# Kernel optimization log

Hardware: AMD Instinct MI355X
Metric: run time of the kernel (lower is better)

The kernel has to match this reference:

```python
import jax, jax.numpy as jnp
import numpy as np

ENC, DEC, B, S = 1024, 1024, 32, 2048


def setup_inputs() -> dict:
    key = jax.random.key(0)
    k1, k2, k3, k4, k5, k6 = jax.random.split(key, 6)
    scale_attn = 1.0 / np.sqrt(ENC + DEC)
    return {
        "decoder_hidden": jax.random.normal(k1, (B, DEC), dtype=jnp.float32),
        "encoder_outputs": jax.random.normal(k2, (B, S, ENC), dtype=jnp.float32),
        "mask": jax.random.randint(k3, (B, S), 0, 2, dtype=jnp.int32),
        "W_attn": jax.random.normal(k4, (ENC + DEC, DEC), dtype=jnp.float32) * scale_attn,
        "b_attn": jax.random.normal(k5, (DEC,), dtype=jnp.float32) * 0.02,
        "v_w": jax.random.normal(k6, (DEC,), dtype=jnp.float32) * (1.0 / np.sqrt(DEC)),
    }


def reference(decoder_hidden, encoder_outputs, mask, W_attn, b_attn, v_w):
    # Split cat((dec_exp, enc)) @ W into two GEMMs (same math, no repeat/concat).
    dec_dim = decoder_hidden.shape[-1]
    W_dec = W_attn[:dec_dim]      # [DEC, DEC]
    W_enc = W_attn[dec_dim:]      # [ENC, DEC]
    dec_proj = decoder_hidden @ W_dec                      # [B, DEC]
    enc_proj = jnp.einsum("bse,ed->bsd", encoder_outputs, W_enc)  # [B, S, DEC]
    energy = jnp.tanh(dec_proj[:, None, :] + enc_proj + b_attn)   # [B, S, DEC]
    scores = jnp.einsum("bsd,d->bs", energy, v_w)                 # [B, S]
    scores = jnp.where(mask == 0, -1e9, scores)
    attn_weights = jax.nn.softmax(scores, axis=1)                 # [B, S]
    context = jnp.einsum("bs,bse->be", attn_weights, encoder_outputs)  # [B, ENC]
    return (context, attn_weights)
```

## Files before the change

kernel.cpp:

```cpp
#include <hip/hip_runtime.h>
#include <hip/hip_bf16.h>
#include <cstdint>


#define ENCD 1024
#define DECD 1024
#define BATCH 32
#define SEQ 2048
#define MTOT (BATCH * SEQ)
#define KDIM 1024
#define NDIM 1024

typedef __attribute__((ext_vector_type(4))) float f32x4;
typedef __attribute__((ext_vector_type(8))) __bf16 bf16x8;
typedef __attribute__((ext_vector_type(8))) unsigned short u16x8;

__device__ __forceinline__ unsigned short f2bf(float f) {
  unsigned int u = __builtin_bit_cast(unsigned int, f);
  u += 0x7fffu + ((u >> 16) & 1u);
  return (unsigned short)(u >> 16);
}

__device__ __forceinline__ float bf2f(unsigned short h) {
  return __builtin_bit_cast(float, (unsigned int)h << 16);
}

__device__ __forceinline__ void async_lds16(const unsigned short* g, unsigned short* l) {
  __builtin_amdgcn_global_load_lds(
      (const __attribute__((address_space(1))) unsigned int*)g,
      (__attribute__((address_space(3))) unsigned int*)l, 16, 0, 0);
}

__global__ void conv_bf16_k(const float* __restrict__ src, unsigned short* __restrict__ dst) {
  const long i = ((long)blockIdx.x * 256 + threadIdx.x) * 8;
  const f32x4 f0 = *(const f32x4*)(src + i);
  const f32x4 f1 = *(const f32x4*)(src + i + 4);
  u16x8 v;
  v[0] = f2bf(f0[0]); v[1] = f2bf(f0[1]); v[2] = f2bf(f0[2]); v[3] = f2bf(f0[3]);
  v[4] = f2bf(f1[0]); v[5] = f2bf(f1[1]); v[6] = f2bf(f1[2]); v[7] = f2bf(f1[3]);
  *(u16x8*)(dst + i) = v;
}

__global__ void wt_k(const float* __restrict__ W, unsigned short* __restrict__ Wt) {
  __shared__ unsigned short t[64][65];
  const int k0 = blockIdx.x * 64, n0 = blockIdx.y * 64;
  const int tx = threadIdx.x & 63, ty = threadIdx.x >> 6;
#pragma unroll
  for (int i = 0; i < 16; ++i) {
    const int k = ty + i * 4;
    t[k][tx] = f2bf(W[(long)(DECD + k0 + k) * NDIM + n0 + tx]);
  }
  __syncthreads();
#pragma unroll
  for (int i = 0; i < 16; ++i) {
    const int n = ty + i * 4;
    Wt[(long)(n0 + n) * KDIM + k0 + tx] = t[tx][n];
  }
}

__global__ void dec1_k(const float* __restrict__ dec, const float* __restrict__ W,
                       float* __restrict__ part) {
  const int idx = blockIdx.x * 256 + threadIdx.x;
  const int kc = blockIdx.y;
  const int b = idx >> 10;
  const int n = idx & 1023;
  const float* d = dec + b * DECD + kc * 128;
  const float* w = W + (long)(kc * 128) * NDIM + n;
  float acc = 0.f;
#pragma unroll 8
  for (int k = 0; k < 128; ++k) acc = fmaf(d[k], w[(long)k * NDIM], acc);
  part[kc * 32768 + idx] = acc;
}

__global__ void dec2_k(const float* __restrict__ part, const float* __restrict__ bias,
                       float* __restrict__ dp) {
  const int idx = blockIdx.x * 256 + threadIdx.x;
  float s = bias[idx & 1023];
#pragma unroll
  for (int kc = 0; kc < 8; ++kc) s += part[kc * 32768 + idx];
  dp[idx] = s;
}

__global__ __launch_bounds__(256, 4) void gemm_fast(
    const unsigned short* __restrict__ Abf, const unsigned short* __restrict__ Wt,
    const float* __restrict__ dp, const float* __restrict__ vw,
    float* __restrict__ sp) {
  __shared__ unsigned short sA[128 * 64];
  __shared__ unsigned short sB[128 * 64];

  const int tid = threadIdx.x;
  const int lane = tid & 63;
  const int wave = tid >> 6;
  const int wm = wave >> 1, wn = wave & 1;
  const int quad = lane >> 4;
  const int l15 = lane & 15;

  const int bn = blockIdx.x;
  const int bm = blockIdx.y;
  const int n0 = bn * 128;
  const int row0 = bm * 128;
  const int bidx = bm >> 4;

  const int srow = lane >> 3;
  const int schunk = (lane & 7) ^ srow;

  const f32x4 zz = {0.f, 0.f, 0.f, 0.f};
  f32x4 acc[4][4];
#pragma unroll
  for (int i = 0; i < 4; ++i)
#pragma unroll
    for (int j = 0; j < 4; ++j) acc[i][j] = zz;

  for (int kt = 0; kt < 16; ++kt) {
    const int k0 = kt * 64;
    __syncthreads();
#pragma unroll
    for (int i = 0; i < 4; ++i) {
      const int r = wave * 32 + i * 8 + srow;
      async_lds16(Abf + (size_t)(row0 + r) * KDIM + k0 + schunk * 8,
                  &sA[(wave * 32 + i * 8) * 64]);
      async_lds16(Wt + (size_t)(n0 + r) * KDIM + k0 + schunk * 8,
                  &sB[(wave * 32 + i * 8) * 64]);
    }
    __syncthreads();
#pragma unroll
    for (int h = 0; h < 2; ++h) {
      bf16x8 af[4], bf[4];
      const int slot = ((h * 4 + quad) ^ (l15 & 7)) * 8;
#pragma unroll
      for (int t = 0; t < 4; ++t) {
        af[t] = __builtin_bit_cast(bf16x8, *(const u16x8*)&sA[(wm * 64 + t * 16 + l15) * 64 + slot]);
        bf[t] = __builtin_bit_cast(bf16x8, *(const u16x8*)&sB[(wn * 64 + t * 16 + l15) * 64 + slot]);
      }
#pragma unroll
      for (int mt = 0; mt < 4; ++mt)
#pragma unroll
        for (int nt = 0; nt < 4; ++nt)
          acc[mt][nt] = __builtin_amdgcn_mfma_f32_16x16x32_bf16(
              af[mt], bf[nt], acc[mt][nt], 0, 0, 0);
    }
  }

  float vv[4], dv[4];
#pragma unroll
  for (int nt = 0; nt < 4; ++nt) {
    const int n = n0 + wn * 64 + nt * 16 + l15;
    vv[nt] = vw[n];
    dv[nt] = dp[bidx * NDIM + n];
  }
  float s_arr[4][4];
#pragma unroll
  for (int mt = 0; mt < 4; ++mt) {
#pragma unroll
    for (int r = 0; r < 4; ++r) {
      float s = 0.f;
#pragma unroll
      for (int nt = 0; nt < 4; ++nt) {
        float x = acc[mt][nt][r] + dv[nt];
        x = fminf(fmaxf(x, -10.f), 10.f);
        const float e = __expf(2.f * x);
        s += (e - 1.f) * __builtin_amdgcn_rcpf(e + 1.f) * vv[nt];
      }
      s += __shfl_xor(s, 1);
      s += __shfl_xor(s, 2);
      s += __shfl_xor(s, 4);
      s += __shfl_xor(s, 8);
      s_arr[mt][r] = s;
    }
  }
  __syncthreads();
  float* sRed = (float*)sA;
  if (wn == 1 && l15 == 0) {
#pragma unroll
    for (int mt = 0; mt < 4; ++mt)
#pragma unroll
      for (int r = 0; r < 4; ++r)
        sRed[wm * 64 + mt * 16 + quad * 4 + r] = s_arr[mt][r];
  }
  __syncthreads();
  if (wn == 0 && l15 == 0) {
#pragma unroll
    for (int mt = 0; mt < 4; ++mt)
#pragma unroll
      for (int r = 0; r < 4; ++r) {
        const int ml = wm * 64 + mt * 16 + quad * 4 + r;
        sp[(size_t)bn * MTOT + row0 + ml] = s_arr[mt][r] + sRed[ml];
      }
  }
}

__global__ void softmax_part_k(const float* __restrict__ sp, const int* __restrict__ mask,
                               float* __restrict__ attn) {
  const int b = blockIdx.x;
  const int tid = threadIdx.x;
  const int w = tid >> 6;
  __shared__ float redm[4], reds[4];
  const int* mrow = mask + b * SEQ;
  float vals[8];
  float mx = -3.0e38f;
#pragma unroll
  for (int i = 0; i < 8; ++i) {
    const int s = tid + i * 256;
    float v = 0.f;
#pragma unroll
    for (int bn = 0; bn < 8; ++bn) v += sp[(size_t)bn * MTOT + b * SEQ + s];
    if (mrow[s] == 0) v = -1.0e9f;
    vals[i] = v;
    mx = fmaxf(mx, v);
  }
#pragma unroll
  for (int off = 1; off < 64; off <<= 1) mx = fmaxf(mx, __shfl_xor(mx, off));
  if ((tid & 63) == 0) redm[w] = mx;
  __syncthreads();
  mx = fmaxf(fmaxf(redm[0], redm[1]), fmaxf(redm[2], redm[3]));
  float sum = 0.f;
#pragma unroll
  for (int i = 0; i < 8; ++i) {
    vals[i] = __expf(vals[i] - mx);
    sum += vals[i];
  }
#pragma unroll
  for (int off = 1; off < 64; off <<= 1) sum += __shfl_xor(sum, off);
  if ((tid & 63) == 0) reds[w] = sum;
  __syncthreads();
  sum = reds[0] + reds[1] + reds[2] + reds[3];
  const float inv = 1.0f / sum;
#pragma unroll
  for (int i = 0; i < 8; ++i) attn[b * SEQ + tid + i * 256] = vals[i] * inv;
}

__global__ void ctx1_k(const float* __restrict__ attn, const unsigned short* __restrict__ Abf,
                       float* __restrict__ part) {
  const int sc = blockIdx.x;
  const int b = blockIdx.y;
  const int e0 = threadIdx.x * 8;
  const float* arow = attn + b * SEQ + sc * 128;
  const unsigned short* base = Abf + (size_t)(b * SEQ + sc * 128) * ENCD + e0;
  float acc[8] = {0.f, 0.f, 0.f, 0.f, 0.f, 0.f, 0.f, 0.f};
#pragma unroll 8
  for (int s = 0; s < 128; ++s) {
    const float w = arow[s];
    const u16x8 v = *(const u16x8*)(base + (size_t)s * ENCD);
#pragma unroll
    for (int j = 0; j < 8; ++j) acc[j] = fmaf(w, bf2f(v[j]), acc[j]);
  }
  float* dst = part + (size_t)sc * (BATCH * ENCD) + b * ENCD + e0;
  *(f32x4*)dst = *(f32x4*)&acc[0];
  *(f32x4*)(dst + 4) = *(f32x4*)&acc[4];
}

__global__ void ctx2_k(const float* __restrict__ part, float* __restrict__ ctx) {
  const int i = blockIdx.x * 256 + threadIdx.x;
  float s = 0.f;
#pragma unroll
  for (int c = 0; c < 16; ++c) s += part[(size_t)c * (BATCH * ENCD) + i];
  ctx[i] = s;
}

__global__ void dec_proj_k2(const float* __restrict__ dec, const float* __restrict__ W,
                            float* __restrict__ dp) {
  const int idx = blockIdx.x * 256 + threadIdx.x;
  const int kc = blockIdx.y;
  const int b = idx >> 10;
  const int n = idx & 1023;
  const float* d = dec + b * DECD + kc * 128;
  const float* w = W + (long)(kc * 128) * NDIM + n;
  float acc = 0.f;
#pragma unroll 8
  for (int k = 0; k < 128; ++k) acc = fmaf(d[k], w[(long)k * NDIM], acc);
  atomicAdd(&dp[idx], acc);
}

__global__ __launch_bounds__(256, 3) void gemm_scores_bf16(
    const unsigned short* __restrict__ Abf, const unsigned short* __restrict__ Wt,
    const float* __restrict__ dp, const float* __restrict__ bias,
    const float* __restrict__ vw, float* __restrict__ scores) {
  __shared__ unsigned short sA[128 * 64];
  __shared__ unsigned short sB[128 * 64];
  const int tid = threadIdx.x;
  const int lane = tid & 63;
  const int wave = tid >> 6;
  const int wm = wave >> 1, wn = wave & 1;
  const int quad = lane >> 4;
  const int l15 = lane & 15;
  const int bn = blockIdx.x, bm = blockIdx.y;
  const int n0 = bn * 128, row0 = bm * 128, bidx = bm >> 4;
  const int srow = lane >> 3;
  const int schunk = (lane & 7) ^ srow;
  const f32x4 zz = {0.f, 0.f, 0.f, 0.f};
  f32x4 acc[4][4];
#pragma unroll
  for (int i = 0; i < 4; ++i)
#pragma unroll
    for (int j = 0; j < 4; ++j) acc[i][j] = zz;
  for (int kt = 0; kt < 16; ++kt) {
    const int k0 = kt * 64;
    __syncthreads();
#pragma unroll
    for (int i = 0; i < 4; ++i) {
      const int r = wave * 32 + i * 8 + srow;
      async_lds16(Abf + (size_t)(row0 + r) * KDIM + k0 + schunk * 8,
                  &sA[(wave * 32 + i * 8) * 64]);
      async_lds16(Wt + (size_t)(n0 + r) * KDIM + k0 + schunk * 8,
                  &sB[(wave * 32 + i * 8) * 64]);
    }
    __syncthreads();
#pragma unroll
    for (int h = 0; h < 2; ++h) {
      bf16x8 af[4], bf[4];
      const int slot = ((h * 4 + quad) ^ (l15 & 7)) * 8;
#pragma unroll
      for (int t = 0; t < 4; ++t) {
        af[t] = __builtin_bit_cast(bf16x8, *(const u16x8*)&sA[(wm * 64 + t * 16 + l15) * 64 + slot]);
        bf[t] = __builtin_bit_cast(bf16x8, *(const u16x8*)&sB[(wn * 64 + t * 16 + l15) * 64 + slot]);
      }
#pragma unroll
      for (int mt = 0; mt < 4; ++mt)
#pragma unroll
        for (int nt = 0; nt < 4; ++nt)
          acc[mt][nt] = __builtin_amdgcn_mfma_f32_16x16x32_bf16(
              af[mt], bf[nt], acc[mt][nt], 0, 0, 0);
    }
  }
  float vv[4], dv[4];
#pragma unroll
  for (int nt = 0; nt < 4; ++nt) {
    const int n = n0 + wn * 64 + nt * 16 + l15;
    vv[nt] = vw[n];
    dv[nt] = dp[bidx * NDIM + n] + bias[n];
  }
#pragma unroll
  for (int mt = 0; mt < 4; ++mt) {
#pragma unroll
    for (int r = 0; r < 4; ++r) {
      float s = 0.f;
#pragma unroll
      for (int nt = 0; nt < 4; ++nt) {
        float x = acc[mt][nt][r] + dv[nt];
        x = fminf(fmaxf(x, -10.f), 10.f);
        const float e = __expf(2.f * x);
        s += (e - 1.f) * __builtin_amdgcn_rcpf(e + 1.f) * vv[nt];
      }
      s += __shfl_xor(s, 1);
      s += __shfl_xor(s, 2);
      s += __shfl_xor(s, 4);
      s += __shfl_xor(s, 8);
      if (l15 == 0) atomicAdd(&scores[row0 + wm * 64 + mt * 16 + quad * 4 + r], s);
    }
  }
}

__global__ __launch_bounds__(256, 2) void gemm_scores_f32(
    const float* __restrict__ Ag, const unsigned short* __restrict__ Wt,
    const float* __restrict__ dp, const float* __restrict__ bias,
    const float* __restrict__ vw, float* __restrict__ scores) {
  __shared__ unsigned short sA[128 * 64];
  __shared__ unsigned short sB[128 * 64];
  const int tid = threadIdx.x;
  const int lane = tid & 63;
  const int wave = tid >> 6;
  const int wm = wave >> 1, wn = wave & 1;
  const int quad = lane >> 4;
  const int l15 = lane & 15;
  const int bn = blockIdx.x, bm = blockIdx.y;
  const int n0 = bn * 128, row0 = bm * 128, bidx = bm >> 4;
  const int sr = tid >> 3, sc = tid & 7;
  const f32x4 zz = {0.f, 0.f, 0.f, 0.f};
  f32x4 acc[4][4];
#pragma unroll
  for (int i = 0; i < 4; ++i)
#pragma unroll
    for (int j = 0; j < 4; ++j) acc[i][j] = zz;
  for (int kt = 0; kt < 16; ++kt) {
    const int k0 = kt * 64;
    __syncthreads();
#pragma unroll
    for (int j = 0; j < 4; ++j) {
      const int r = sr + 32 * j;
      const int c = sc ^ (r & 7);
      const float* src = Ag + (long)(row0 + r) * KDIM + (k0 + c * 8);
      f32x4 f0 = *(const f32x4*)src;
      f32x4 f1 = *(const f32x4*)(src + 4);
      u16x8 v;
      v[0] = f2bf(f0[0]); v[1] = f2bf(f0[1]); v[2] = f2bf(f0[2]); v[3] = f2bf(f0[3]);
      v[4] = f2bf(f1[0]); v[5] = f2bf(f1[1]); v[6] = f2bf(f1[2]); v[7] = f2bf(f1[3]);
      *(u16x8*)&sA[r * 64 + sc * 8] = v;
      *(u16x8*)&sB[r * 64 + sc * 8] = *(const u16x8*)(Wt + (long)(n0 + r) * KDIM + (k0 + c * 8));
    }
    __syncthreads();
#pragma unroll
    for (int h = 0; h < 2; ++h) {
      const int cs = ((h * 4 + quad) ^ (lane & 7)) * 8;
      bf16x8 af[4], bf[4];
#pragma unroll
      for (int t = 0; t < 4; ++t) {
        af[t] = __builtin_bit_cast(bf16x8, *(const u16x8*)&sA[(wm * 64 + t * 16 + l15) * 64 + cs]);
        bf[t] = __builtin_bit_cast(bf16x8, *(const u16x8*)&sB[(wn * 64 + t * 16 + l15) * 64 + cs]);
      }
#pragma unroll
      for (int mt = 0; mt < 4; ++mt)
#pragma unroll
        for (int nt = 0; nt < 4; ++nt)
          acc[mt][nt] = __builtin_amdgcn_mfma_f32_16x16x32_bf16(
              af[mt], bf[nt], acc[mt][nt], 0, 0, 0);
    }
  }
  float vv[4], dv[4];
#pragma unroll
  for (int nt = 0; nt < 4; ++nt) {
    const int n = n0 + wn * 64 + nt * 16 + l15;
    vv[nt] = vw[n];
    dv[nt] = dp[bidx * NDIM + n] + bias[n];
  }
#pragma unroll
  for (int mt = 0; mt < 4; ++mt) {
#pragma unroll
    for (int r = 0; r < 4; ++r) {
      float s = 0.f;
#pragma unroll
      for (int nt = 0; nt < 4; ++nt) {
        float x = acc[mt][nt][r] + dv[nt];
        x = fminf(fmaxf(x, -10.f), 10.f);
        const float e = __expf(2.f * x);
        s += (e - 1.f) * __builtin_amdgcn_rcpf(e + 1.f) * vv[nt];
      }
      s += __shfl_xor(s, 1);
      s += __shfl_xor(s, 2);
      s += __shfl_xor(s, 4);
      s += __shfl_xor(s, 8);
      if (l15 == 0) atomicAdd(&scores[row0 + wm * 64 + mt * 16 + quad * 4 + r], s);
    }
  }
}

__global__ void softmax_k(float* __restrict__ sc, const int* __restrict__ mask) {
  const int b = blockIdx.x;
  const int tid = threadIdx.x;
  const int w = tid >> 6;
  __shared__ float redm[4], reds[4];
  float* row = sc + b * SEQ;
  const int* mrow = mask + b * SEQ;
  float vals[8];
  float mx = -3.0e38f;
#pragma unroll
  for (int i = 0; i < 8; ++i) {
    const int s = tid + i * 256;
    float v = row[s];
    if (mrow[s] == 0) v = -1.0e9f;
    vals[i] = v;
    mx = fmaxf(mx, v);
  }
#pragma unroll
  for (int off = 1; off < 64; off <<= 1) mx = fmaxf(mx, __shfl_xor(mx, off));
  if ((tid & 63) == 0) redm[w] = mx;
  __syncthreads();
  mx = fmaxf(fmaxf(redm[0], redm[1]), fmaxf(redm[2], redm[3]));
  float sum = 0.f;
#pragma unroll
  for (int i = 0; i < 8; ++i) {
    vals[i] = __expf(vals[i] - mx);
    sum += vals[i];
  }
#pragma unroll
  for (int off = 1; off < 64; off <<= 1) sum += __shfl_xor(sum, off);
  if ((tid & 63) == 0) reds[w] = sum;
  __syncthreads();
  sum = reds[0] + reds[1] + reds[2] + reds[3];
  const float inv = 1.0f / sum;
#pragma unroll
  for (int i = 0; i < 8; ++i) row[tid + i * 256] = vals[i] * inv;
}

__global__ void context_k(const float* __restrict__ attn, const float* __restrict__ enc,
                          float* __restrict__ ctx) {
  const int b = blockIdx.y;
  const int s0 = blockIdx.x * 32;
  const int e = threadIdx.x * 4;
  const float* arow = attn + b * SEQ + s0;
  const float* ebase = enc + (long)(b * SEQ + s0) * ENCD + e;
  f32x4 acc = {0.f, 0.f, 0.f, 0.f};
#pragma unroll 8
  for (int s = 0; s < 32; ++s) {
    const float w = arow[s];
    const f32x4 v = *(const f32x4*)(ebase + (long)s * ENCD);
    acc += w * v;
  }
  float* dst = ctx + b * ENCD + e;
  atomicAdd(dst + 0, acc[0]);
  atomicAdd(dst + 1, acc[1]);
  atomicAdd(dst + 2, acc[2]);
  atomicAdd(dst + 3, acc[3]);
}

extern "C" void kernel_launch(void* const* d_in, const int* in_sizes, int n_in,
                              void* d_out, int out_size, void* d_ws, size_t ws_size,
                              hipStream_t stream) {
  (void)in_sizes; (void)n_in; (void)out_size;
  const float* dec  = (const float*)d_in[0];
  const float* enc  = (const float*)d_in[1];
  const int*   mask = (const int*)d_in[2];
  const float* W    = (const float*)d_in[3];
  const float* bias = (const float*)d_in[4];
  const float* vw   = (const float*)d_in[5];

  float* ctx  = (float*)d_out;
  float* attn = (float*)d_out + BATCH * ENCD;
  unsigned short* Wt  = (unsigned short*)d_ws;
  unsigned short* Abf = (unsigned short*)((char*)d_ws + (2ull << 20));
  float* shared = (float*)((char*)d_ws + (130ull << 20));

  const size_t needA = (132ull << 20);
  const size_t needB = (2ull << 20) + ((size_t)MTOT * KDIM * 2);

  wt_k<<<dim3(16, 16), 256, 0, stream>>>(W, Wt);
  if (ws_size >= needA) {
    dec1_k<<<dim3(128, 8), 256, 0, stream>>>(dec, W, shared);
    dec2_k<<<128, 256, 0, stream>>>(shared, bias, ctx);
    conv_bf16_k<<<32768, 256, 0, stream>>>(enc, Abf);
    gemm_fast<<<dim3(8, 512), 256, 0, stream>>>(Abf, Wt, ctx, vw, shared);
    softmax_part_k<<<32, 256, 0, stream>>>(shared, mask, attn);
    ctx1_k<<<dim3(16, 32), 128, 0, stream>>>(attn, Abf, shared);
    ctx2_k<<<128, 256, 0, stream>>>(shared, ctx);
  } else if (ws_size >= needB) {
    hipMemsetAsync(attn, 0, (size_t)MTOT * sizeof(float), stream);
    hipMemsetAsync(ctx, 0, (size_t)(BATCH * NDIM) * sizeof(float), stream);
    dec_proj_k2<<<dim3(128, 8), 256, 0, stream>>>(dec, W, ctx);
    conv_bf16_k<<<32768, 256, 0, stream>>>(enc, Abf);
    gemm_scores_bf16<<<dim3(8, 512), 256, 0, stream>>>(Abf, Wt, ctx, bias, vw, attn);
    softmax_k<<<32, 256, 0, stream>>>(attn, mask);
    hipMemsetAsync(ctx, 0, (size_t)(BATCH * ENCD) * sizeof(float), stream);
    context_k<<<dim3(64, 32), 256, 0, stream>>>(attn, enc, ctx);
  } else {
    hipMemsetAsync(attn, 0, (size_t)MTOT * sizeof(float), stream);
    hipMemsetAsync(ctx, 0, (size_t)(BATCH * NDIM) * sizeof(float), stream);
    dec_proj_k2<<<dim3(128, 8), 256, 0, stream>>>(dec, W, ctx);
    gemm_scores_f32<<<dim3(8, 512), 256, 0, stream>>>(enc, Wt, ctx, bias, vw, attn);
    softmax_k<<<32, 256, 0, stream>>>(attn, mask);
    hipMemsetAsync(ctx, 0, (size_t)(BATCH * ENCD) * sizeof(float), stream);
    context_k<<<dim3(64, 32), 256, 0, stream>>>(attn, enc, ctx);
  }
}
```

Before: 572.6 us.

## Use 256x256 double-buffered 8-wave GEMM tile with interleaved async loads

Replaces the 128x128 single-buffered GEMM with a 256x256 tile run by 8 waves. It double-buffers LDS and interleaves async global-to-LDS loads with MFMA phases, using explicit vmcnt waits and s_setprio. This is meant to hide load latency, which the old loop exposed behind __syncthreads, and to halve the global re-reads of A and W. The larger tile uses 128KB of LDS and more accumulator registers, which limits occupancy. Separately, ctx1_k is split across two halves of the sequence per block to raise parallelism.

After: 595.8 us. 1.04x slower.

```diff
diff --git a/kernel.cpp b/kernel.cpp
--- a/kernel.cpp
+++ b/kernel.cpp
@@ -29,6 +29,22 @@
   __builtin_amdgcn_global_load_lds(
       (const __attribute__((address_space(1))) unsigned int*)g,
       (__attribute__((address_space(3))) unsigned int*)l, 16, 0, 0);
+}
+
+__device__ __forceinline__ void barx() {
+  __builtin_amdgcn_s_barrier();
+  asm volatile("" ::: "memory");
+}
+
+template <int N>
+__device__ __forceinline__ void waitv() {
+  if constexpr (N == 0) {
+    asm volatile("s_waitcnt vmcnt(0)" ::: "memory");
+  } else if constexpr (N == 2) {
+    asm volatile("s_waitcnt vmcnt(2)" ::: "memory");
+  } else {
+    asm volatile("s_waitcnt vmcnt(4)" ::: "memory");
+  }
 }
 
 __global__ void conv_bf16_k(const float* __restrict__ src, unsigned short* __restrict__ dst) {
@@ -81,65 +97,159 @@
   dp[idx] = s;
 }
 
-__global__ __launch_bounds__(256, 4) void gemm_fast(
+template <bool STG, int W1, int W2>
+__device__ __forceinline__ void gtile(
+    const unsigned short* Acur, const unsigned short* Bcur,
+    unsigned short* Anxt, unsigned short* Bnxt,
+    const unsigned short* Ab, const unsigned short* Bb, int k0n,
+    int wm, int wn, int wv, int quad, int l15, int srow, int schunk,
+    f32x4 (&acc)[8][4], bf16x8 (&aF)[4][2], bf16x8 (&bF)[4][2]) {
+  const int sw = l15 & 7;
+#define RDF(buf, row, h) \
+  __builtin_bit_cast(bf16x8, *(const u16x8*)&(buf)[(row) * 64 + ((((h) * 4 + quad) ^ sw) * 8)])
+#pragma unroll
+  for (int mt = 0; mt < 4; ++mt) {
+    const int row = wm * 128 + mt * 16 + l15;
+    aF[mt][0] = RDF(Acur, row, 0);
+    aF[mt][1] = RDF(Acur, row, 1);
+  }
+#pragma unroll
+  for (int nt = 0; nt < 2; ++nt) {
+    const int row = wn * 64 + nt * 16 + l15;
+    bF[nt][0] = RDF(Bcur, row, 0);
+    bF[nt][1] = RDF(Bcur, row, 1);
+  }
+  if (STG) {
+    async_lds16(Bb + (size_t)(wv * 16 + srow) * KDIM + k0n + schunk * 8, Bnxt + (wv * 16) * 64);
+    async_lds16(Bb + (size_t)(wv * 16 + 8 + srow) * KDIM + k0n + schunk * 8, Bnxt + (wv * 16 + 8) * 64);
+  }
+  barx();
+  __builtin_amdgcn_s_setprio(1);
+#pragma unroll
+  for (int h = 0; h < 2; ++h)
+#pragma unroll
+    for (int mt = 0; mt < 4; ++mt)
+#pragma unroll
+      for (int nt = 0; nt < 2; ++nt)
+        acc[mt][nt] = __builtin_amdgcn_mfma_f32_16x16x32_bf16(aF[mt][h], bF[nt][h], acc[mt][nt], 0, 0, 0);
+  __builtin_amdgcn_s_setprio(0);
+  barx();
+#pragma unroll
+  for (int nt = 2; nt < 4; ++nt) {
+    const int row = wn * 64 + nt * 16 + l15;
+    bF[nt][0] = RDF(Bcur, row, 0);
+    bF[nt][1] = RDF(Bcur, row, 1);
+  }
+  if (STG) {
+    async_lds16(Bb + (size_t)(128 + wv * 16 + srow) * KDIM + k0n + schunk * 8, Bnxt + (128 + wv * 16) * 64);
+    async_lds16(Bb + (size_t)(128 + wv * 16 + 8 + srow) * KDIM + k0n + schunk * 8, Bnxt + (128 + wv * 16 + 8) * 64);
+  }
+  waitv<W1>();
+  barx();
+  __builtin_amdgcn_s_setprio(1);
+#pragma unroll
+  for (int h = 0; h < 2; ++h)
+#pragma unroll
+    for (int mt = 0; mt < 4; ++mt)
+#pragma unroll
+      for (int nt = 0; nt < 2; ++nt)
+        acc[mt][2 + nt] = __builtin_amdgcn_mfma_f32_16x16x32_bf16(aF[mt][h], bF[2 + nt][h], acc[mt][2 + nt], 0, 0, 0);
+  __builtin_amdgcn_s_setprio(0);
+  barx();
+#pragma unroll
+  for (int mt = 0; mt < 4; ++mt) {
+    const int row = wm * 128 + (4 + mt) * 16 + l15;
+    aF[mt][0] = RDF(Acur, row, 0);
+    aF[mt][1] = RDF(Acur, row, 1);
+  }
+  if (STG) {
+    async_lds16(Ab + (size_t)(wv * 8 + srow) * KDIM + k0n + schunk * 8, Anxt + (wv * 8) * 64);
+    async_lds16(Ab + (size_t)(128 + wv * 8 + srow) * KDIM + k0n + schunk * 8, Anxt + (128 + wv * 8) * 64);
+  }
+  barx();
+  __builtin_amdgcn_s_setprio(1);
+#pragma unroll
+  for (int h = 0; h < 2; ++h)
+#pragma unroll
+    for (int mt = 0; mt < 4; ++mt)
+#pragma unroll
+      for (int nt = 0; nt < 2; ++nt)
+        acc[4 + mt][nt] = __builtin_amdgcn_mfma_f32_16x16x32_bf16(aF[mt][h], bF[nt][h], acc[4 + mt][nt], 0, 0, 0);
+  __builtin_amdgcn_s_setprio(0);
+  barx();
+  if (STG) {
+    async_lds16(Ab + (size_t)(64 + wv * 8 + srow) * KDIM + k0n + schunk * 8, Anxt + (64 + wv * 8) * 64);
+    async_lds16(Ab + (size_t)(192 + wv * 8 + srow) * KDIM + k0n + schunk * 8, Anxt + (192 + wv * 8) * 64);
+  }
+  waitv<W2>();
+  barx();
+  __builtin_amdgcn_s_setprio(1);
+#pragma unroll
+  for (int h = 0; h < 2; ++h)
+#pragma unroll
+    for (int mt = 0; mt < 4; ++mt)
+#pragma unroll
+      for (int nt = 0; nt < 2; ++nt)
+        acc[4 + mt][2 + nt] = __builtin_amdgcn_mfma_f32_16x16x32_bf16(aF[mt][h], bF[2 + nt][h], acc[4 + mt][2 + nt], 0, 0, 0);
+  __builtin_amdgcn_s_setprio(0);
+  barx();
+#undef RDF
+}
+
+__global__ __launch_bounds__(512, 2) void gemm8_k(
     const unsigned short* __restrict__ Abf, const unsigned short* __restrict__ Wt,
     const float* __restrict__ dp, const float* __restrict__ vw,
     float* __restrict__ sp) {
-  __shared__ unsigned short sA[128 * 64];
-  __shared__ unsigned short sB[128 * 64];
-
+  __shared__ unsigned short sA[2][256 * 64];
+  __shared__ unsigned short sB[2][256 * 64];
   const int tid = threadIdx.x;
   const int lane = tid & 63;
-  const int wave = tid >> 6;
-  const int wm = wave >> 1, wn = wave & 1;
+  const int wv = tid >> 6;
+  const int wm = wv >> 2, wn = wv & 3;
   const int quad = lane >> 4;
   const int l15 = lane & 15;
+  const int srow = lane >> 3;
+  const int schunk = (lane & 7) ^ srow;
 
   const int bn = blockIdx.x;
   const int bm = blockIdx.y;
-  const int n0 = bn * 128;
-  const int row0 = bm * 128;
-  const int bidx = bm >> 4;
-
-  const int srow = lane >> 3;
-  const int schunk = (lane & 7) ^ srow;
+  const int n0 = bn * 256;
+  const int row0 = bm * 256;
+  const int bidx = bm >> 3;
+
+  const unsigned short* Ab = Abf + (size_t)row0 * KDIM;
+  const unsigned short* Bb = Wt + (size_t)n0 * KDIM;
 
   const f32x4 zz = {0.f, 0.f, 0.f, 0.f};
-  f32x4 acc[4][4];
-#pragma unroll
-  for (int i = 0; i < 4; ++i)
+  f32x4 acc[8][4];
+#pragma unroll
+  for (int i = 0; i < 8; ++i)
 #pragma unroll
     for (int j = 0; j < 4; ++j) acc[i][j] = zz;
-
-  for (int kt = 0; kt < 16; ++kt) {
-    const int k0 = kt * 64;
-    __syncthreads();
-#pragma unroll
-    for (int i = 0; i < 4; ++i) {
-      const int r = wave * 32 + i * 8 + srow;
-      async_lds16(Abf + (size_t)(row0 + r) * KDIM + k0 + schunk * 8,
-                  &sA[(wave * 32 + i * 8) * 64]);
-      async_lds16(Wt + (size_t)(n0 + r) * KDIM + k0 + schunk * 8,
-                  &sB[(wave * 32 + i * 8) * 64]);
-    }
-    __syncthreads();
-#pragma unroll
-    for (int h = 0; h < 2; ++h) {
-      bf16x8 af[4], bf[4];
-      const int slot = ((h * 4 + quad) ^ (l15 & 7)) * 8;
-#pragma unroll
-      for (int t = 0; t < 4; ++t) {
-        af[t] = __builtin_bit_cast(bf16x8, *(const u16x8*)&sA[(wm * 64 + t * 16 + l15) * 64 + slot]);
-        bf[t] = __builtin_bit_cast(bf16x8, *(const u16x8*)&sB[(wn * 64 + t * 16 + l15) * 64 + slot]);
-      }
-#pragma unroll
-      for (int mt = 0; mt < 4; ++mt)
-#pragma unroll
-        for (int nt = 0; nt < 4; ++nt)
-          acc[mt][nt] = __builtin_amdgcn_mfma_f32_16x16x32_bf16(
-              af[mt], bf[nt], acc[mt][nt], 0, 0, 0);
-    }
-  }
+  bf16x8 aF[4][2], bF[4][2];
+
+  async_lds16(Bb + (size_t)(wv * 16 + srow) * KDIM + schunk * 8, &sB[0][(wv * 16) * 64]);
+  async_lds16(Bb + (size_t)(wv * 16 + 8 + srow) * KDIM + schunk * 8, &sB[0][(wv * 16 + 8) * 64]);
+  async_lds16(Bb + (size_t)(128 + wv * 16 + srow) * KDIM + schunk * 8, &sB[0][(128 + wv * 16) * 64]);
+  async_lds16(Bb + (size_t)(128 + wv * 16 + 8 + srow) * KDIM + schunk * 8, &sB[0][(128 + wv * 16 + 8) * 64]);
+  async_lds16(Ab + (size_t)(wv * 8 + srow) * KDIM + schunk * 8, &sA[0][(wv * 8) * 64]);
+  async_lds16(Ab + (size_t)(128 + wv * 8 + srow) * KDIM + schunk * 8, &sA[0][(128 + wv * 8) * 64]);
+  async_lds16(Ab + (size_t)(64 + wv * 8 + srow) * KDIM + schunk * 8, &sA[0][(64 + wv * 8) * 64]);
+  async_lds16(Ab + (size_t)(192 + wv * 8 + srow) * KDIM + schunk * 8, &sA[0][(192 + wv * 8) * 64]);
+  waitv<2>();
+  barx();
+
+  for (int it = 0; it < 7; ++it) {
+    const int kb = it * 2;
+    gtile<true, 4, 2>(sA[0], sB[0], sA[1], sB[1], Ab, Bb, (kb + 1) * 64,
+                      wm, wn, wv, quad, l15, srow, schunk, acc, aF, bF);
+    gtile<true, 4, 2>(sA[1], sB[1], sA[0], sB[0], Ab, Bb, (kb + 2) * 64,
+                      wm, wn, wv, quad, l15, srow, schunk, acc, aF, bF);
+  }
+  gtile<true, 4, 2>(sA[0], sB[0], sA[1], sB[1], Ab, Bb, 15 * 64,
+                    wm, wn, wv, quad, l15, srow, schunk, acc, aF, bF);
+  gtile<false, 0, 0>(sA[1], sB[1], sA[0], sB[0], Ab, Bb, 0,
+                     wm, wn, wv, quad, l15, srow, schunk, acc, aF, bF);
 
   float vv[4], dv[4];
 #pragma unroll
@@ -148,9 +258,9 @@
     vv[nt] = vw[n];
     dv[nt] = dp[bidx * NDIM + n];
   }
-  float s_arr[4][4];
-#pragma unroll
-  for (int mt = 0; mt < 4; ++mt) {
+  float* sRed = (float*)sA;
+#pragma unroll
+  for (int mt = 0; mt < 8; ++mt) {
 #pragma unroll
     for (int r = 0; r < 4; ++r) {
       float s = 0.f;
@@ -165,27 +275,13 @@
       s += __shfl_xor(s, 2);
       s += __shfl_xor(s, 4);
       s += __shfl_xor(s, 8);
-      s_arr[mt][r] = s;
+      if (l15 == 0) sRed[wn * 256 + wm * 128 + mt * 16 + quad * 4 + r] = s;
     }
   }
   __syncthreads();
-  float* sRed = (float*)sA;
-  if (wn == 1 && l15 == 0) {
-#pragma unroll
-    for (int mt = 0; mt < 4; ++mt)
-#pragma unroll
-      for (int r = 0; r < 4; ++r)
-        sRed[wm * 64 + mt * 16 + quad * 4 + r] = s_arr[mt][r];
-  }
-  __syncthreads();
-  if (wn == 0 && l15 == 0) {
-#pragma unroll
-    for (int mt = 0; mt < 4; ++mt)
-#pragma unroll
-      for (int r = 0; r < 4; ++r) {
-        const int ml = wm * 64 + mt * 16 + quad * 4 + r;
-        sp[(size_t)bn * MTOT + row0 + ml] = s_arr[mt][r] + sRed[ml];
-      }
+  if (tid < 256) {
+    const float s4 = sRed[tid] + sRed[256 + tid] + sRed[512 + tid] + sRed[768 + tid];
+    sp[(size_t)bn * MTOT + row0 + tid] = s4;
   }
 }
 
@@ -203,7 +299,7 @@
     const int s = tid + i * 256;
     float v = 0.f;
 #pragma unroll
-    for (int bn = 0; bn < 8; ++bn) v += sp[(size_t)bn * MTOT + b * SEQ + s];
+    for (int bn = 0; bn < 4; ++bn) v += sp[(size_t)bn * MTOT + b * SEQ + s];
     if (mrow[s] == 0) v = -1.0e9f;
     vals[i] = v;
     mx = fmaxf(mx, v);
@@ -231,22 +327,35 @@
 
 __global__ void ctx1_k(const float* __restrict__ attn, const unsigned short* __restrict__ Abf,
                        float* __restrict__ part) {
+  __shared__ float red[128 * 8];
   const int sc = blockIdx.x;
   const int b = blockIdx.y;
-  const int e0 = threadIdx.x * 8;
-  const float* arow = attn + b * SEQ + sc * 128;
-  const unsigned short* base = Abf + (size_t)(b * SEQ + sc * 128) * ENCD + e0;
+  const int half = threadIdx.x >> 7;
+  const int te = threadIdx.x & 127;
+  const int e0 = te * 8;
+  const int sbase = sc * 128 + half * 64;
+  const float* arow = attn + b * SEQ + sbase;
+  const unsigned short* base = Abf + (size_t)(b * SEQ + sbase) * ENCD + e0;
   float acc[8] = {0.f, 0.f, 0.f, 0.f, 0.f, 0.f, 0.f, 0.f};
 #pragma unroll 8
-  for (int s = 0; s < 128; ++s) {
+  for (int s = 0; s < 64; ++s) {
     const float w = arow[s];
     const u16x8 v = *(const u16x8*)(base + (size_t)s * ENCD);
 #pragma unroll
     for (int j = 0; j < 8; ++j) acc[j] = fmaf(w, bf2f(v[j]), acc[j]);
   }
-  float* dst = part + (size_t)sc * (BATCH * ENCD) + b * ENCD + e0;
-  *(f32x4*)dst = *(f32x4*)&acc[0];
-  *(f32x4*)(dst + 4) = *(f32x4*)&acc[4];
+  if (half == 1) {
+#pragma unroll
+    for (int j = 0; j < 8; ++j) red[te * 8 + j] = acc[j];
+  }
+  __syncthreads();
+  if (half == 0) {
+#pragma unroll
+    for (int j = 0; j < 8; ++j) acc[j] += red[te * 8 + j];
+    float* dst = part + (size_t)sc * (BATCH * ENCD) + b * ENCD + e0;
+    *(f32x4*)dst = *(f32x4*)&acc[0];
+    *(f32x4*)(dst + 4) = *(f32x4*)&acc[4];
+  }
 }
 
 __global__ void ctx2_k(const float* __restrict__ part, float* __restrict__ ctx) {
@@ -517,9 +626,9 @@
     dec1_k<<<dim3(128, 8), 256, 0, stream>>>(dec, W, shared);
     dec2_k<<<128, 256, 0, stream>>>(shared, bias, ctx);
     conv_bf16_k<<<32768, 256, 0, stream>>>(enc, Abf);
-    gemm_fast<<<dim3(8, 512), 256, 0, stream>>>(Abf, Wt, ctx, vw, shared);
+    gemm8_k<<<dim3(4, 256), 512, 0, stream>>>(Abf, Wt, ctx, vw, shared);
     softmax_part_k<<<32, 256, 0, stream>>>(shared, mask, attn);
-    ctx1_k<<<dim3(16, 32), 128, 0, stream>>>(attn, Abf, shared);
+    ctx1_k<<<dim3(16, 32), 256, 0, stream>>>(attn, Abf, shared);
     ctx2_k<<<128, 256, 0, stream>>>(shared, ctx);
   } else if (ws_size >= needB) {
     hipMemsetAsync(attn, 0, (size_t)MTOT * sizeof(float), stream);
```

## Fuse prep kernels, remap GEMM tiles across XCDs, fuse softmax with context

Applied to the files above, without the earlier changes.

Merges the weight transpose, decoder projection (now one block per output chunk with the full K loop) and the fp32-to-bf16 conversion of the encoder outputs into a single heterogeneous prep kernel. It also remaps the GEMM block index so consecutive row tiles land on the same XCD for L2 reuse. Finally it fuses softmax with the context reduction: each block recomputes the softmax for its batch row and reduces one 128-wide slice of the context in shared memory, which removes the partial buffers and extra launches. The trade-offs are that softmax is computed redundantly 8 times per batch row, and the decoder projection now runs a serial 1024-long dot product per thread.

Result: slower. 595.1 us (+3.9%).

```diff
diff --git a/kernel.cpp b/kernel.cpp
--- a/kernel.cpp
+++ b/kernel.cpp
@@ -58,27 +58,51 @@
   }
 }
 
-__global__ void dec1_k(const float* __restrict__ dec, const float* __restrict__ W,
-                       float* __restrict__ part) {
-  const int idx = blockIdx.x * 256 + threadIdx.x;
-  const int kc = blockIdx.y;
-  const int b = idx >> 10;
-  const int n = idx & 1023;
-  const float* d = dec + b * DECD + kc * 128;
-  const float* w = W + (long)(kc * 128) * NDIM + n;
-  float acc = 0.f;
+__global__ __launch_bounds__(256) void prep_k(
+    const float* __restrict__ dec, const float* __restrict__ enc,
+    const float* __restrict__ W, const float* __restrict__ bias,
+    float* __restrict__ dp, unsigned short* __restrict__ Wt,
+    unsigned short* __restrict__ Abf) {
+  const int gb = blockIdx.x;
+  const int tid = threadIdx.x;
+  if (gb < 128) {
+    const int b = gb >> 2;
+    const int n = (gb & 3) * 256 + tid;
+    const float* d = dec + b * DECD;
+    const float* w = W + n;
+    float acc = bias[n];
 #pragma unroll 8
-  for (int k = 0; k < 128; ++k) acc = fmaf(d[k], w[(long)k * NDIM], acc);
-  part[kc * 32768 + idx] = acc;
-}
-
-__global__ void dec2_k(const float* __restrict__ part, const float* __restrict__ bias,
-                       float* __restrict__ dp) {
-  const int idx = blockIdx.x * 256 + threadIdx.x;
-  float s = bias[idx & 1023];
-#pragma unroll
-  for (int kc = 0; kc < 8; ++kc) s += part[kc * 32768 + idx];
-  dp[idx] = s;
+    for (int k = 0; k < 1024; ++k) acc = fmaf(d[k], w[(size_t)k * NDIM], acc);
+    dp[b * NDIM + n] = acc;
+  } else if (gb < 384) {
+    __shared__ unsigned short t[64][65];
+    const int g2 = gb - 128;
+    const int k0 = (g2 & 15) * 64, n0 = (g2 >> 4) * 64;
+    const int tx = tid & 63, ty = tid >> 6;
+#pragma unroll
+    for (int i = 0; i < 16; ++i) {
+      const int k = ty + i * 4;
+      t[k][tx] = f2bf(W[(size_t)(DECD + k0 + k) * NDIM + n0 + tx]);
+    }
+    __syncthreads();
+#pragma unroll
+    for (int i = 0; i < 16; ++i) {
+      const int n = ty + i * 4;
+      Wt[(size_t)(n0 + n) * KDIM + k0 + tx] = t[tx][n];
+    }
+  } else {
+    const int cb = gb - 384;
+#pragma unroll
+    for (int k = 0; k < 16; ++k) {
+      const long i = (((long)cb + (long)k * 2048) * 256 + tid) * 8;
+      const f32x4 f0 = *(const f32x4*)(enc + i);
+      const f32x4 f1 = *(const f32x4*)(enc + i + 4);
+      u16x8 v;
+      v[0] = f2bf(f0[0]); v[1] = f2bf(f0[1]); v[2] = f2bf(f0[2]); v[3] = f2bf(f0[3]);
+      v[4] = f2bf(f1[0]); v[5] = f2bf(f1[1]); v[6] = f2bf(f1[2]); v[7] = f2bf(f1[3]);
+      *(u16x8*)(Abf + i) = v;
+    }
+  }
 }
 
 __global__ __launch_bounds__(256, 4) void gemm_fast(
@@ -95,8 +119,11 @@
   const int quad = lane >> 4;
   const int l15 = lane & 15;
 
-  const int bn = blockIdx.x;
-  const int bm = blockIdx.y;
+  const int f = blockIdx.x + (blockIdx.y << 3);
+  const int xcd = f & 7;
+  const int c = f >> 3;
+  const int bn = c & 7;
+  const int bm = xcd + ((c >> 3) << 3);
   const int n0 = bn * 128;
   const int row0 = bm * 128;
   const int bidx = bm >> 4;
@@ -189,12 +216,17 @@
   }
 }
 
-__global__ void softmax_part_k(const float* __restrict__ sp, const int* __restrict__ mask,
-                               float* __restrict__ attn) {
-  const int b = blockIdx.x;
+__global__ __launch_bounds__(256) void sm_ctx_k(
+    const float* __restrict__ sp, const int* __restrict__ mask,
+    const unsigned short* __restrict__ Abf,
+    float* __restrict__ attn, float* __restrict__ ctx) {
+  __shared__ float a_s[SEQ];
+  __shared__ float red[16][16][8];
+  __shared__ float redm[4], reds[4];
+  const int ec = blockIdx.x;
+  const int b = blockIdx.y;
   const int tid = threadIdx.x;
   const int w = tid >> 6;
-  __shared__ float redm[4], reds[4];
   const int* mrow = mask + b * SEQ;
   float vals[8];
   float mx = -3.0e38f;
@@ -203,7 +235,7 @@
     const int s = tid + i * 256;
     float v = 0.f;
 #pragma unroll
-    for (int bn = 0; bn < 8; ++bn) v += sp[(size_t)bn * MTOT + b * SEQ + s];
+    for (int p = 0; p < 8; ++p) v += sp[(size_t)p * MTOT + b * SEQ + s];
     if (mrow[s] == 0) v = -1.0e9f;
     vals[i] = v;
     mx = fmaxf(mx, v);
@@ -226,35 +258,34 @@
   sum = reds[0] + reds[1] + reds[2] + reds[3];
   const float inv = 1.0f / sum;
 #pragma unroll
-  for (int i = 0; i < 8; ++i) attn[b * SEQ + tid + i * 256] = vals[i] * inv;
-}
-
-__global__ void ctx1_k(const float* __restrict__ attn, const unsigned short* __restrict__ Abf,
-                       float* __restrict__ part) {
-  const int sc = blockIdx.x;
-  const int b = blockIdx.y;
-  const int e0 = threadIdx.x * 8;
-  const float* arow = attn + b * SEQ + sc * 128;
-  const unsigned short* base = Abf + (size_t)(b * SEQ + sc * 128) * ENCD + e0;
+  for (int i = 0; i < 8; ++i) {
+    const float av = vals[i] * inv;
+    a_s[tid + i * 256] = av;
+    if (ec == 0) attn[b * SEQ + tid + i * 256] = av;
+  }
+  __syncthreads();
+  const int sg = tid >> 4, es = tid & 15;
+  const int e0 = ec * 128 + es * 8;
+  const unsigned short* base = Abf + (size_t)(b * SEQ) * ENCD + e0;
   float acc[8] = {0.f, 0.f, 0.f, 0.f, 0.f, 0.f, 0.f, 0.f};
-#pragma unroll 8
-  for (int s = 0; s < 128; ++s) {
-    const float w = arow[s];
+#pragma unroll 4
+  for (int k = 0; k < 128; ++k) {
+    const int s = sg + k * 16;
+    const float wgt = a_s[s];
     const u16x8 v = *(const u16x8*)(base + (size_t)s * ENCD);
 #pragma unroll
-    for (int j = 0; j < 8; ++j) acc[j] = fmaf(w, bf2f(v[j]), acc[j]);
-  }
-  float* dst = part + (size_t)sc * (BATCH * ENCD) + b * ENCD + e0;
-  *(f32x4*)dst = *(f32x4*)&acc[0];
-  *(f32x4*)(dst + 4) = *(f32x4*)&acc[4];
-}
-
-__global__ void ctx2_k(const float* __restrict__ part, float* __restrict__ ctx) {
-  const int i = blockIdx.x * 256 + threadIdx.x;
-  float s = 0.f;
-#pragma unroll
-  for (int c = 0; c < 16; ++c) s += part[(size_t)c * (BATCH * ENCD) + i];
-  ctx[i] = s;
+    for (int j = 0; j < 8; ++j) acc[j] = fmaf(wgt, bf2f(v[j]), acc[j]);
+  }
+#pragma unroll
+  for (int j = 0; j < 8; ++j) red[sg][es][j] = acc[j];
+  __syncthreads();
+  if (tid < 128) {
+    const int es2 = tid >> 3, j = tid & 7;
+    float ssum = 0.f;
+#pragma unroll
+    for (int g = 0; g < 16; ++g) ssum += red[g][es2][j];
+    ctx[b * ENCD + ec * 128 + es2 * 8 + j] = ssum;
+  }
 }
 
 __global__ void dec_proj_k2(const float* __restrict__ dec, const float* __restrict__ W,
@@ -512,16 +543,12 @@
   const size_t needA = (132ull << 20);
   const size_t needB = (2ull << 20) + ((size_t)MTOT * KDIM * 2);
 
-  wt_k<<<dim3(16, 16), 256, 0, stream>>>(W, Wt);
   if (ws_size >= needA) {
-    dec1_k<<<dim3(128, 8), 256, 0, stream>>>(dec, W, shared);
-    dec2_k<<<128, 256, 0, stream>>>(shared, bias, ctx);
-    conv_bf16_k<<<32768, 256, 0, stream>>>(enc, Abf);
+    prep_k<<<384 + 2048, 256, 0, stream>>>(dec, enc, W, bias, ctx, Wt, Abf);
     gemm_fast<<<dim3(8, 512), 256, 0, stream>>>(Abf, Wt, ctx, vw, shared);
-    softmax_part_k<<<32, 256, 0, stream>>>(shared, mask, attn);
-    ctx1_k<<<dim3(16, 32), 128, 0, stream>>>(attn, Abf, shared);
-    ctx2_k<<<128, 256, 0, stream>>>(shared, ctx);
+    sm_ctx_k<<<dim3(8, 32), 256, 0, stream>>>(shared, mask, Abf, attn, ctx);
   } else if (ws_size >= needB) {
+    wt_k<<<dim3(16, 16), 256, 0, stream>>>(W, Wt);
     hipMemsetAsync(attn, 0, (size_t)MTOT * sizeof(float), stream);
     hipMemsetAsync(ctx, 0, (size_t)(BATCH * NDIM) * sizeof(float), stream);
     dec_proj_k2<<<dim3(128, 8), 256, 0, stream>>>(dec, W, ctx);
@@ -531,6 +558,7 @@
     hipMemsetAsync(ctx, 0, (size_t)(BATCH * ENCD) * sizeof(float), stream);
     context_k<<<dim3(64, 32), 256, 0, stream>>>(attn, enc, ctx);
   } else {
+    wt_k<<<dim3(16, 16), 256, 0, stream>>>(W, Wt);
     hipMemsetAsync(attn, 0, (size_t)MTOT * sizeof(float), stream);
     hipMemsetAsync(ctx, 0, (size_t)(BATCH * NDIM) * sizeof(float), stream);
     dec_proj_k2<<<dim3(128, 8), 256, 0, stream>>>(dec, W, ctx);
```
